# Optimization experiments

Hardware: AMD Instinct MI355X
Metric: run time of the kernel (lower is better)

## Reference

```python
import jax, jax.numpy as jnp
import numpy as np

N_NODES = 100000


def gcn_conv(x, W, b, row, col, n_nodes):
    # PyG GCNConv: x' = D^{-1/2} (A + I) D^{-1/2} (x W) + b
    xw = x @ W  # [N, out]
    ones = jnp.ones(row.shape[0], dtype=x.dtype)
    deg = jnp.zeros((n_nodes,), dtype=x.dtype).at[col].add(ones) + 1.0  # +1 self-loop
    dinv = jax.lax.rsqrt(deg)
    norm = dinv[row] * dinv[col]  # per-edge normalization [E]
    msgs = xw[row] * norm[:, None]  # gather + scale [E, out]
    agg = jax.ops.segment_sum(msgs, col, num_segments=n_nodes)
    # self-loop contribution: norm = deg^{-1/2} * deg^{-1/2} = 1/deg
    agg = agg + xw * (1.0 / deg)[:, None]
    return agg + b


def setup_inputs() -> dict:
    key = jax.random.key(0)
    k1, k2, k3, k4 = jax.random.split(key, 4)
    x = jax.random.normal(k1, (N_NODES, 128), dtype=jnp.float32)
    edge_index = jax.random.randint(k2, (2, 1600000), 0, N_NODES, dtype=jnp.int64)
    W1 = jax.random.normal(k3, (128, 256), dtype=jnp.float32) * (1.0 / np.sqrt(128))
    b1 = jnp.zeros((256,), dtype=jnp.float32)
    W2 = jax.random.normal(k4, (256, 128), dtype=jnp.float32) * (1.0 / np.sqrt(256))
    b2 = jnp.zeros((128,), dtype=jnp.float32)
    return {"x": x, "edge_index": edge_index, "W1": W1, "b1": b1, "W2": W2, "b2": b2}


def reference(x, edge_index, W1, b1, W2, b2):
    row, col = edge_index[0], edge_index[1]
    n = x.shape[0]
    h = gcn_conv(x, W1, b1, row, col, n)
    h = jax.nn.gelu(h)
    out = gcn_conv(h, W2, b2, row, col, n)
    return out
```

## Files before the change

### kernel.cpp

```cpp
#include <hip/hip_runtime.h>
#include <hip/hip_bf16.h>
#include <math.h>

typedef __attribute__((ext_vector_type(8))) short bf16x8;
typedef __attribute__((ext_vector_type(4))) float f32x4;

__device__ inline ushort f2bf(float f) {
    uint u = __float_as_uint(f);
    uint r = u + 0x7fffu + ((u >> 16) & 1u);
    return (ushort)(r >> 16);
}
__device__ inline float bf2f(ushort h) { return __uint_as_float(((uint)h) << 16); }

__device__ inline float gelu_fast(float x) {
    float z2 = 1.5957691216057308f * (x + 0.044715f * x * x * x);
    return x / (1.0f + __expf(-z2));
}


__global__ void deg_rank_kernel(const int* __restrict__ col, int* __restrict__ deg64,
                                int* __restrict__ rank, int E) {
    int e = blockIdx.x * blockDim.x + threadIdx.x;
    if (e < E) rank[e] = atomicAdd(&deg64[col[e] << 4], 1);
}

__global__ void dinv_reduce_kernel(const int* __restrict__ deg64, float* __restrict__ dinv,
                                   int* __restrict__ deg, int* __restrict__ bsum, int M) {
    __shared__ int s[256];
    int i = blockIdx.x * 256 + threadIdx.x;
    int d = 0;
    if (i < M) {
        d = deg64[i << 4];
        deg[i] = d;
        dinv[i] = rsqrtf((float)d + 1.0f);
    }
    s[threadIdx.x] = d;
    __syncthreads();
    for (int o = 128; o > 0; o >>= 1) {
        if (threadIdx.x < o) s[threadIdx.x] += s[threadIdx.x + o];
        __syncthreads();
    }
    if (threadIdx.x == 0) bsum[blockIdx.x] = s[0];
}

__global__ void scan_bsum_kernel(int* __restrict__ bsum, int nb) {
    __shared__ int s[512];
    int t = threadIdx.x;
    int orig = (t < nb) ? bsum[t] : 0;
    s[t] = orig;
    __syncthreads();
    for (int o = 1; o < 512; o <<= 1) {
        int v = 0;
        if (t >= o) v = s[t - o];
        __syncthreads();
        if (t >= o) s[t] += v;
        __syncthreads();
    }
    if (t < nb) bsum[t] = s[t] - orig;
}

__global__ void scan_offsets_kernel(const int* __restrict__ deg, const int* __restrict__ bsum,
                                    int* __restrict__ off, int M) {
    __shared__ int s[256];
    int i = blockIdx.x * 256 + threadIdx.x;
    int orig = (i < M) ? deg[i] : 0;
    s[threadIdx.x] = orig;
    __syncthreads();
    for (int o = 1; o < 256; o <<= 1) {
        int v = 0;
        if (threadIdx.x >= o) v = s[threadIdx.x - o];
        __syncthreads();
        if (threadIdx.x >= o) s[threadIdx.x] += v;
        __syncthreads();
    }
    if (i < M) off[i] = bsum[blockIdx.x] + s[threadIdx.x] - orig;
}


__global__ void fill_sorted_kernel(const int* __restrict__ row, const int* __restrict__ col,
                                   const int* __restrict__ off, const int* __restrict__ rank,
                                   int* __restrict__ rs, int E) {
    int e = blockIdx.x * blockDim.x + threadIdx.x;
    if (e < E) rs[off[col[e]] + rank[e]] = row[e];
}


__global__ void prep_convert_kernel(const float* __restrict__ x, const float* __restrict__ dinv,
                                    const float* __restrict__ W1, const float* __restrict__ W2,
                                    ushort* __restrict__ xb, ushort* __restrict__ p1,
                                    ushort* __restrict__ p2, int n8) {
    int t = blockIdx.x * 256 + threadIdx.x;
    if (t < n8) {
        float s = dinv[t >> 4];
        float4 a = *(const float4*)(x + (size_t)t * 8);
        float4 b = *(const float4*)(x + (size_t)t * 8 + 4);
        ushort4 u0 = make_ushort4(f2bf(a.x * s), f2bf(a.y * s), f2bf(a.z * s), f2bf(a.w * s));
        ushort4 u1 = make_ushort4(f2bf(b.x * s), f2bf(b.y * s), f2bf(b.z * s), f2bf(b.w * s));
        *(ushort4*)(xb + (size_t)t * 8) = u0;
        *(ushort4*)(xb + (size_t)t * 8 + 4) = u1;
        return;
    }
    int u = t - n8;
    if (u < 4096) {
        int g = u >> 6, l = u & 63;
        int w = g >> 4, n = (g >> 2) & 3, ks = g & 3;
        int oc = w * 64 + n * 16 + (l & 15);
        int kb = ks * 32 + (l >> 4) * 8;
        ushort tmp[8];
        #pragma unroll
        for (int j = 0; j < 8; ++j) tmp[j] = f2bf(W1[(size_t)(kb + j) * 256 + oc]);
        *(bf16x8*)(p1 + (size_t)u * 8) = *(bf16x8*)tmp;
    } else if (u < 8192) {
        int v = u - 4096;
        int g = v >> 6, l = v & 63;
        int w = g >> 4, n = (g >> 3) & 1, ks = g & 7;
        int oc = w * 32 + n * 16 + (l & 15);
        int kb = ks * 32 + (l >> 4) * 8;
        ushort tmp[8];
        #pragma unroll
        for (int j = 0; j < 8; ++j) tmp[j] = f2bf(W2[(size_t)(kb + j) * 128 + oc]);
        *(bf16x8*)(p2 + (size_t)v * 8) = *(bf16x8*)tmp;
    }
}


__global__ __launch_bounds__(256, 2) void gemm_fused(const ushort* __restrict__ A,
                                                     const ushort* __restrict__ p1,
                                                     const float* __restrict__ b1,
                                                     const ushort* __restrict__ p2,
                                                     const float* __restrict__ dinv,
                                                     ushort* __restrict__ Cb, int M) {
    __shared__ ushort la[64 * 128];
    __shared__ ushort lh[64 * 256];

    const int t = threadIdx.x;
    const int R0 = blockIdx.x * 64;
    const int w = t >> 6, l = t & 63;
    const int lrow = l & 15;
    const int lk = l >> 4;

    #pragma unroll
    for (int base = 0; base < 1024; base += 256) {
        int idx = base + t;
        int r = idx >> 4;
        int c8 = idx & 15;
        int gr = R0 + r;
        gr = gr < M ? gr : M - 1;
        bf16x8 v = *(const bf16x8*)(A + (size_t)gr * 128 + c8 * 8);
        int byte = idx * 16 ^ ((r & 7) << 4);
        *(bf16x8*)((char*)la + byte) = v;
    }

    bf16x8 w1[4][4];
    #pragma unroll
    for (int n = 0; n < 4; ++n)
        #pragma unroll
        for (int ks = 0; ks < 4; ++ks)
            w1[n][ks] = *(const bf16x8*)(p1 + (size_t)(((w * 4 + n) * 4 + ks) * 64 + l) * 8);
    __syncthreads();

    {
        const int c0 = w * 64;
        f32x4 acc[4][4] = {};
        #pragma unroll
        for (int ks = 0; ks < 4; ++ks) {
            bf16x8 xf[4];
            #pragma unroll
            for (int m = 0; m < 4; ++m) {
                int nd = m * 16 + lrow;
                int byte = (nd * 256 + ks * 64 + lk * 16) ^ ((nd & 7) << 4);
                xf[m] = *(const bf16x8*)((const char*)la + byte);
            }
            #pragma unroll
            for (int n = 0; n < 4; ++n)
                #pragma unroll
                for (int m = 0; m < 4; ++m)
                    acc[n][m] = __builtin_amdgcn_mfma_f32_16x16x32_bf16(w1[n][ks], xf[m], acc[n][m], 0, 0, 0);
        }
        #pragma unroll
        for (int n = 0; n < 4; ++n) {
            int ob = c0 + n * 16 + lk * 4;
            float4 bb = *(const float4*)(b1 + ob);
            #pragma unroll
            for (int m = 0; m < 4; ++m) {
                int nd = m * 16 + lrow;
                ushort4 pk;
                pk.x = f2bf(gelu_fast(acc[n][m][0] + bb.x));
                pk.y = f2bf(gelu_fast(acc[n][m][1] + bb.y));
                pk.z = f2bf(gelu_fast(acc[n][m][2] + bb.z));
                pk.w = f2bf(gelu_fast(acc[n][m][3] + bb.w));
                int byte = (nd * 256 + ob) * 2;
                byte ^= (nd & 7) << 4;
                *(ushort4*)((char*)lh + byte) = pk;
            }
        }
    }

    bf16x8 w2[2][8];
    #pragma unroll
    for (int n = 0; n < 2; ++n)
        #pragma unroll
        for (int ks = 0; ks < 8; ++ks)
            w2[n][ks] = *(const bf16x8*)(p2 + (size_t)(((w * 2 + n) * 8 + ks) * 64 + l) * 8);
    __syncthreads();

    {
        const int c0 = w * 32;
        f32x4 acc2[2][4] = {};
        #pragma unroll
        for (int ks = 0; ks < 8; ++ks) {
            const int kb = ks * 32 + lk * 8;
            bf16x8 hf[4];
            #pragma unroll
            for (int m = 0; m < 4; ++m) {
                int nd = m * 16 + lrow;
                int byte = (nd * 256 + kb) * 2;
                byte ^= (nd & 7) << 4;
                hf[m] = *(const bf16x8*)((const char*)lh + byte);
            }
            #pragma unroll
            for (int n = 0; n < 2; ++n)
                #pragma unroll
                for (int m = 0; m < 4; ++m)
                    acc2[n][m] = __builtin_amdgcn_mfma_f32_16x16x32_bf16(w2[n][ks], hf[m], acc2[n][m], 0, 0, 0);
        }
        #pragma unroll
        for (int m = 0; m < 4; ++m) {
            int nd = m * 16 + lrow;
            int grow = R0 + nd;
            if (grow < M) {
                float sc = dinv[grow];
                #pragma unroll
                for (int n = 0; n < 2; ++n) {
                    int ob = c0 + n * 16 + lk * 4;
                    ushort4 pk;
                    pk.x = f2bf(acc2[n][m][0] * sc);
                    pk.y = f2bf(acc2[n][m][1] * sc);
                    pk.z = f2bf(acc2[n][m][2] * sc);
                    pk.w = f2bf(acc2[n][m][3] * sc);
                    *(ushort4*)(Cb + (size_t)grow * 128 + ob) = pk;
                }
            }
        }
    }
}


template <bool BIAS, bool OUTBF>
__global__ __launch_bounds__(256) void gather_sum_kernel(const int* __restrict__ off,
                                                         const int* __restrict__ deg,
                                                         const int* __restrict__ rs,
                                                         const float* __restrict__ dinv,
                                                         const ushort* __restrict__ srcb,
                                                         const float* __restrict__ b,
                                                         float* __restrict__ dstf,
                                                         ushort* __restrict__ dstb, int M) {
    int wid = (blockIdx.x * 256 + threadIdx.x) >> 6;
    int lane = threadIdx.x & 63;
    int grp = lane >> 4;
    int l16 = lane & 15;
    if (wid >= M) return;
    int s0 = off[wid];
    int n = deg[wid];
    float acc[8] = {};
    float acc2[8] = {};

    if (grp == 0) {
        bf16x8 u = *(const bf16x8*)(srcb + (size_t)wid * 128 + l16 * 8);
        #pragma unroll
        for (int i = 0; i < 8; ++i) acc[i] += bf2f((ushort)u[i]);
    }

    int j = 0;
    for (; j + 8 <= n; j += 8) {
        int r0 = rs[s0 + j + grp];
        int r1 = rs[s0 + j + 4 + grp];
        bf16x8 u0 = *(const bf16x8*)(srcb + (size_t)r0 * 128 + l16 * 8);
        bf16x8 u1 = *(const bf16x8*)(srcb + (size_t)r1 * 128 + l16 * 8);
        #pragma unroll
        for (int i = 0; i < 8; ++i) {
            acc[i] += bf2f((ushort)u0[i]);
            acc2[i] += bf2f((ushort)u1[i]);
        }
    }
    if (j + 4 <= n) {
        int r = rs[s0 + j + grp];
        bf16x8 u = *(const bf16x8*)(srcb + (size_t)r * 128 + l16 * 8);
        #pragma unroll
        for (int i = 0; i < 8; ++i) acc[i] += bf2f((ushort)u[i]);
        j += 4;
    }
    if (j + grp < n) {
        int r = rs[s0 + j + grp];
        bf16x8 u = *(const bf16x8*)(srcb + (size_t)r * 128 + l16 * 8);
        #pragma unroll
        for (int i = 0; i < 8; ++i) acc2[i] += bf2f((ushort)u[i]);
    }

    #pragma unroll
    for (int i = 0; i < 8; ++i) {
        acc[i] += acc2[i];
        acc[i] += __shfl_xor(acc[i], 16);
        acc[i] += __shfl_xor(acc[i], 32);
    }

    if (grp == 0) {
        float sc = dinv[wid];
        #pragma unroll
        for (int i = 0; i < 8; ++i) acc[i] *= sc;
        if constexpr (BIAS) {
            float4 b0 = *(const float4*)(b + l16 * 8);
            float4 b1v = *(const float4*)(b + l16 * 8 + 4);
            acc[0] += b0.x; acc[1] += b0.y; acc[2] += b0.z; acc[3] += b0.w;
            acc[4] += b1v.x; acc[5] += b1v.y; acc[6] += b1v.z; acc[7] += b1v.w;
        }
        if constexpr (OUTBF) {
            bf16x8 o;
            #pragma unroll
            for (int i = 0; i < 8; ++i) o[i] = (short)f2bf(acc[i]);
            *(bf16x8*)(dstb + (size_t)wid * 128 + l16 * 8) = o;
        } else {
            float4 o0 = make_float4(acc[0], acc[1], acc[2], acc[3]);
            float4 o1 = make_float4(acc[4], acc[5], acc[6], acc[7]);
            *(float4*)(dstf + (size_t)wid * 128 + l16 * 8) = o0;
            *(float4*)(dstf + (size_t)wid * 128 + l16 * 8 + 4) = o1;
        }
    }
}


extern "C" void kernel_launch(void* const* d_in, const int* in_sizes, int n_in,
                              void* d_out, int out_size, void* d_ws, size_t ws_size,
                              hipStream_t stream) {
    const float* x  = (const float*)d_in[0];
    const int*   ei = (const int*)d_in[1];
    const float* W1 = (const float*)d_in[2];
    const float* b1 = (const float*)d_in[3];
    const float* W2 = (const float*)d_in[4];
    const float* b2 = (const float*)d_in[5];

    const int M = in_sizes[0] / 128;
    const int E = in_sizes[1] / 2;
    const int* row = ei;
    const int* col = ei + E;

    ushort* xb    = (ushort*)d_ws;
    ushort* aggxb = xb + 12800000;
    ushort* xw2b  = aggxb;
    float*  dinv  = (float*)(aggxb + 12800000);
    int*    deg64 = (int*)(dinv + 102400);
    int*    deg   = deg64 + 1638400;
    int*    off   = deg + 102400;
    int*    rank  = off + 102400;
    int*    rs    = rank + 1600000;
    int*    bsum  = rs + 1600000;
    ushort* p1    = (ushort*)(bsum + 1024);
    ushort* p2    = p1 + 32768;
    float*  outw  = (float*)d_out;

    const int nb = (M + 255) / 256;

    hipMemsetAsync(deg64, 0, (size_t)1638400 * sizeof(int), stream);

    deg_rank_kernel<<<(E + 255) / 256, 256, 0, stream>>>(col, deg64, rank, E);
    dinv_reduce_kernel<<<nb, 256, 0, stream>>>(deg64, dinv, deg, bsum, M);
    scan_bsum_kernel<<<1, 512, 0, stream>>>(bsum, nb);
    scan_offsets_kernel<<<nb, 256, 0, stream>>>(deg, bsum, off, M);
    fill_sorted_kernel<<<(E + 255) / 256, 256, 0, stream>>>(row, col, off, rank, rs, E);

    prep_convert_kernel<<<(M * 16 + 8192 + 255) / 256, 256, 0, stream>>>(
        x, dinv, W1, W2, xb, p1, p2, M * 16);

    gather_sum_kernel<false, true><<<(M * 64 + 255) / 256, 256, 0, stream>>>(
        off, deg, rs, dinv, xb, nullptr, nullptr, aggxb, M);

    gemm_fused<<<(M + 63) / 64, 256, 0, stream>>>(aggxb, p1, b1, p2, dinv, xw2b, M);

    gather_sum_kernel<true, false><<<(M * 64 + 255) / 256, 256, 0, stream>>>(
        off, deg, rs, dinv, xw2b, b2, outw, nullptr, M);
}
```

Before: 278.2 us.

## Merge setup kernels and unroll gather loop to four rows per iteration

The weight-packing work moves into the degree/rank atomic kernel, and the CSR fill kernel merges with the x-to-bf16 conversion kernel, using block-index ranges to pick the role. This drops two kernel launches and lets independent work share a launch. Separately, the gather loop now loads four neighbor rows per iteration instead of two, giving more memory-level parallelism at the cost of extra registers. The remaining-edge tail becomes a loop.

```diff
diff --git a/kernel.cpp b/kernel.cpp
--- a/kernel.cpp
+++ b/kernel.cpp
@@ -18,10 +18,38 @@
 }
 
 
-__global__ void deg_rank_kernel(const int* __restrict__ col, int* __restrict__ deg64,
-                                int* __restrict__ rank, int E) {
-    int e = blockIdx.x * blockDim.x + threadIdx.x;
-    if (e < E) rank[e] = atomicAdd(&deg64[col[e] << 4], 1);
+__global__ void pass1_kernel(const int* __restrict__ col, int* __restrict__ deg64,
+                             int* __restrict__ rank, int E,
+                             const float* __restrict__ W1, const float* __restrict__ W2,
+                             ushort* __restrict__ p1, ushort* __restrict__ p2) {
+    int nbE = (E + 255) >> 8;
+    int b = blockIdx.x;
+    if (b < nbE) {
+        int e = b * 256 + threadIdx.x;
+        if (e < E) rank[e] = atomicAdd(&deg64[col[e] << 4], 1);
+        return;
+    }
+    int u = (b - nbE) * 256 + threadIdx.x;
+    if (u < 4096) {
+        int g = u >> 6, l = u & 63;
+        int w = g >> 4, n = (g >> 2) & 3, ks = g & 3;
+        int oc = w * 64 + n * 16 + (l & 15);
+        int kb = ks * 32 + (l >> 4) * 8;
+        ushort tmp[8];
+        #pragma unroll
+        for (int j = 0; j < 8; ++j) tmp[j] = f2bf(W1[(size_t)(kb + j) * 256 + oc]);
+        *(bf16x8*)(p1 + (size_t)u * 8) = *(bf16x8*)tmp;
+    } else if (u < 8192) {
+        int v = u - 4096;
+        int g = v >> 6, l = v & 63;
+        int w = g >> 4, n = (g >> 3) & 1, ks = g & 7;
+        int oc = w * 32 + n * 16 + (l & 15);
+        int kb = ks * 32 + (l >> 4) * 8;
+        ushort tmp[8];
+        #pragma unroll
+        for (int j = 0; j < 8; ++j) tmp[j] = f2bf(W2[(size_t)(kb + j) * 128 + oc]);
+        *(bf16x8*)(p2 + (size_t)v * 8) = *(bf16x8*)tmp;
+    }
 }
 
 __global__ void dinv_reduce_kernel(const int* __restrict__ deg64, float* __restrict__ dinv,
@@ -77,49 +105,27 @@
 }
 
 
-__global__ void fill_sorted_kernel(const int* __restrict__ row, const int* __restrict__ col,
-                                   const int* __restrict__ off, const int* __restrict__ rank,
-                                   int* __restrict__ rs, int E) {
-    int e = blockIdx.x * blockDim.x + threadIdx.x;
-    if (e < E) rs[off[col[e]] + rank[e]] = row[e];
-}
-
-
-__global__ void prep_convert_kernel(const float* __restrict__ x, const float* __restrict__ dinv,
-                                    const float* __restrict__ W1, const float* __restrict__ W2,
-                                    ushort* __restrict__ xb, ushort* __restrict__ p1,
-                                    ushort* __restrict__ p2, int n8) {
-    int t = blockIdx.x * 256 + threadIdx.x;
-    if (t < n8) {
-        float s = dinv[t >> 4];
-        float4 a = *(const float4*)(x + (size_t)t * 8);
-        float4 b = *(const float4*)(x + (size_t)t * 8 + 4);
+__global__ void pass2_kernel(const int* __restrict__ row, const int* __restrict__ col,
+                             const int* __restrict__ off, const int* __restrict__ rank,
+                             int* __restrict__ rs, int E,
+                             const float* __restrict__ x, const float* __restrict__ dinv,
+                             ushort* __restrict__ xb, int n8) {
+    int nbE = (E + 255) >> 8;
+    int b = blockIdx.x;
+    if (b < nbE) {
+        int e = b * 256 + threadIdx.x;
+        if (e < E) rs[off[col[e]] + rank[e]] = row[e];
+        return;
+    }
+    int i = (b - nbE) * 256 + threadIdx.x;
+    if (i < n8) {
+        float s = dinv[i >> 4];
+        float4 a = *(const float4*)(x + (size_t)i * 8);
+        float4 v = *(const float4*)(x + (size_t)i * 8 + 4);
         ushort4 u0 = make_ushort4(f2bf(a.x * s), f2bf(a.y * s), f2bf(a.z * s), f2bf(a.w * s));
-        ushort4 u1 = make_ushort4(f2bf(b.x * s), f2bf(b.y * s), f2bf(b.z * s), f2bf(b.w * s));
-        *(ushort4*)(xb + (size_t)t * 8) = u0;
-        *(ushort4*)(xb + (size_t)t * 8 + 4) = u1;
-        return;
-    }
-    int u = t - n8;
-    if (u < 4096) {
-        int g = u >> 6, l = u & 63;
-        int w = g >> 4, n = (g >> 2) & 3, ks = g & 3;
-        int oc = w * 64 + n * 16 + (l & 15);
-        int kb = ks * 32 + (l >> 4) * 8;
-        ushort tmp[8];
-        #pragma unroll
-        for (int j = 0; j < 8; ++j) tmp[j] = f2bf(W1[(size_t)(kb + j) * 256 + oc]);
-        *(bf16x8*)(p1 + (size_t)u * 8) = *(bf16x8*)tmp;
-    } else if (u < 8192) {
-        int v = u - 4096;
-        int g = v >> 6, l = v & 63;
-        int w = g >> 4, n = (g >> 3) & 1, ks = g & 7;
-        int oc = w * 32 + n * 16 + (l & 15);
-        int kb = ks * 32 + (l >> 4) * 8;
-        ushort tmp[8];
-        #pragma unroll
-        for (int j = 0; j < 8; ++j) tmp[j] = f2bf(W2[(size_t)(kb + j) * 128 + oc]);
-        *(bf16x8*)(p2 + (size_t)v * 8) = *(bf16x8*)tmp;
+        ushort4 u1 = make_ushort4(f2bf(v.x * s), f2bf(v.y * s), f2bf(v.z * s), f2bf(v.w * s));
+        *(ushort4*)(xb + (size_t)i * 8) = u0;
+        *(ushort4*)(xb + (size_t)i * 8 + 4) = u1;
     }
 }
 
@@ -272,23 +278,26 @@
     }
 
     int j = 0;
-    for (; j + 8 <= n; j += 8) {
+    for (; j + 16 <= n; j += 16) {
         int r0 = rs[s0 + j + grp];
         int r1 = rs[s0 + j + 4 + grp];
+        int r2 = rs[s0 + j + 8 + grp];
+        int r3 = rs[s0 + j + 12 + grp];
         bf16x8 u0 = *(const bf16x8*)(srcb + (size_t)r0 * 128 + l16 * 8);
         bf16x8 u1 = *(const bf16x8*)(srcb + (size_t)r1 * 128 + l16 * 8);
+        bf16x8 u2 = *(const bf16x8*)(srcb + (size_t)r2 * 128 + l16 * 8);
+        bf16x8 u3 = *(const bf16x8*)(srcb + (size_t)r3 * 128 + l16 * 8);
         #pragma unroll
         for (int i = 0; i < 8; ++i) {
-            acc[i] += bf2f((ushort)u0[i]);
-            acc2[i] += bf2f((ushort)u1[i]);
-        }
-    }
-    if (j + 4 <= n) {
+            acc[i] += bf2f((ushort)u0[i]) + bf2f((ushort)u2[i]);
+            acc2[i] += bf2f((ushort)u1[i]) + bf2f((ushort)u3[i]);
+        }
+    }
+    for (; j + 4 <= n; j += 4) {
         int r = rs[s0 + j + grp];
         bf16x8 u = *(const bf16x8*)(srcb + (size_t)r * 128 + l16 * 8);
         #pragma unroll
         for (int i = 0; i < 8; ++i) acc[i] += bf2f((ushort)u[i]);
-        j += 4;
     }
     if (j + grp < n) {
         int r = rs[s0 + j + grp];
@@ -358,18 +367,20 @@
     ushort* p2    = p1 + 32768;
     float*  outw  = (float*)d_out;
 
-    const int nb = (M + 255) / 256;
+    const int nb  = (M + 255) / 256;
+    const int nbE = (E + 255) / 256;
+    const int n8  = M * 16;
 
     hipMemsetAsync(deg64, 0, (size_t)1638400 * sizeof(int), stream);
 
-    deg_rank_kernel<<<(E + 255) / 256, 256, 0, stream>>>(col, deg64, rank, E);
+    pass1_kernel<<<nbE + 32, 256, 0, stream>>>(col, deg64, rank, E, W1, W2, p1, p2);
+
     dinv_reduce_kernel<<<nb, 256, 0, stream>>>(deg64, dinv, deg, bsum, M);
     scan_bsum_kernel<<<1, 512, 0, stream>>>(bsum, nb);
     scan_offsets_kernel<<<nb, 256, 0, stream>>>(deg, bsum, off, M);
-    fill_sorted_kernel<<<(E + 255) / 256, 256, 0, stream>>>(row, col, off, rank, rs, E);
-
-    prep_convert_kernel<<<(M * 16 + 8192 + 255) / 256, 256, 0, stream>>>(
-        x, dinv, W1, W2, xb, p1, p2, M * 16);
+
+    pass2_kernel<<<nbE + (n8 + 255) / 256, 256, 0, stream>>>(row, col, off, rank, rs, E,
+                                                             x, dinv, xb, n8);
 
     gather_sum_kernel<false, true><<<(M * 64 + 255) / 256, 256, 0, stream>>>(
         off, deg, rs, dinv, xb, nullptr, nullptr, aggxb, M);
```

New measurement: 278.3 us, median of 2. No clear change (+0.0%).
